# Performance work log

Hardware: AMD Instinct MI355X
Metric: run time of the kernel (lower is better)

Reference implementation:

```python
import jax, jax.numpy as jnp
import numpy as np

IMG_SHAPE = (256, 256, 256)


def _rot3(a):
    # Rx @ Ry @ Rz, matching _compute_rotation
    ax, ay, az = a[0], a[1], a[2]
    cx, sx = jnp.cos(ax), jnp.sin(ax)
    cy, sy = jnp.cos(ay), jnp.sin(ay)
    cz, sz = jnp.cos(az), jnp.sin(az)
    one = jnp.ones_like(ax)
    zero = jnp.zeros_like(ax)
    Rx = jnp.stack([jnp.stack([one, zero, zero]),
                    jnp.stack([zero, cx, -sx]),
                    jnp.stack([zero, sx, cx])])
    Ry = jnp.stack([jnp.stack([cy, zero, sy]),
                    jnp.stack([zero, one, zero]),
                    jnp.stack([-sy, zero, cy])])
    Rz = jnp.stack([jnp.stack([cz, -sz, zero]),
                    jnp.stack([sz, cz, zero]),
                    jnp.stack([zero, zero, one])])
    return Rx @ Ry @ Rz


def _rigid4(a, t, cog):
    # T_center_inv @ T_trans @ T_rot @ T_center
    R = _rot3(a)
    Tc = jnp.eye(4, dtype=a.dtype).at[:3, 3].set(-cog)
    Tci = jnp.eye(4, dtype=a.dtype).at[:3, 3].set(cog)
    Tt = jnp.eye(4, dtype=a.dtype).at[:3, 3].set(t)
    Tr = jnp.eye(4, dtype=a.dtype).at[:3, :3].set(R)
    return Tci @ Tt @ Tr @ Tc


def _trilinear(vol, di, dj, dk):
    # fast_3D_interp_torch(mode='linear'): trilinear interp, zero outside bounds
    D, H, W = vol.shape
    ok = (di >= 0) & (di <= D - 1) & (dj >= 0) & (dj <= H - 1) & (dk >= 0) & (dk <= W - 1)
    di = jnp.clip(di, 0.0, D - 1)
    dj = jnp.clip(dj, 0.0, H - 1)
    dk = jnp.clip(dk, 0.0, W - 1)
    fi = jnp.floor(di).astype(jnp.int32)
    fj = jnp.floor(dj).astype(jnp.int32)
    fk = jnp.floor(dk).astype(jnp.int32)
    ci = jnp.clip(fi + 1, 0, D - 1)
    cj = jnp.clip(fj + 1, 0, H - 1)
    ck = jnp.clip(fk + 1, 0, W - 1)
    wi = di - fi
    wj = dj - fj
    wk = dk - fk
    out = (vol[fi, fj, fk] * (1 - wi) * (1 - wj) * (1 - wk)
           + vol[fi, fj, ck] * (1 - wi) * (1 - wj) * wk
           + vol[fi, cj, fk] * (1 - wi) * wj * (1 - wk)
           + vol[fi, cj, ck] * (1 - wi) * wj * wk
           + vol[ci, fj, fk] * wi * (1 - wj) * (1 - wk)
           + vol[ci, fj, ck] * wi * (1 - wj) * wk
           + vol[ci, cj, fk] * wi * wj * (1 - wk)
           + vol[ci, cj, ck] * wi * wj * wk)
    return jnp.where(ok, out, jnp.zeros_like(out))


def setup_inputs() -> dict:
    key = jax.random.key(0)
    k1, k2 = jax.random.split(key)
    image_targ = jax.random.normal(k1, (1, 1) + IMG_SHAPE, dtype=jnp.float32)
    # small rotation so most of the warped grid stays in bounds (angle_factor=1)
    angle = 0.1 * jax.random.normal(k2, (1, 3), dtype=jnp.float32)
    translation = jnp.zeros((1, 3), dtype=jnp.float32)
    v2r = np.eye(4, dtype=np.float32)
    v2r[:3, 3] = -127.5  # center-of-volume RAS origin
    ref_v2r = jnp.asarray(v2r)
    flo_v2r = jnp.asarray(v2r)
    cog = jnp.zeros((3,), dtype=jnp.float32)
    return {"image_targ": image_targ, "angle": angle, "translation": translation,
            "ref_v2r": ref_v2r, "flo_v2r": flo_v2r, "cog": cog}


def reference(image_targ, angle, translation, ref_v2r, flo_v2r, cog):
    # tx_factor = angle_factor = 1 -> params used as-is
    T_rig = jax.vmap(lambda a, t: _rigid4(a, t, cog))(angle, translation)  # [B,4,4]
    T = (jnp.linalg.inv(flo_v2r) @ T_rig[0] @ ref_v2r).astype(jnp.float32)
    D, H, W = image_targ.shape[2:]
    gi, gj, gk = jnp.meshgrid(jnp.arange(D, dtype=jnp.float32),
                              jnp.arange(H, dtype=jnp.float32),
                              jnp.arange(W, dtype=jnp.float32), indexing='ij')
    di = T[0, 0] * gi + T[0, 1] * gj + T[0, 2] * gk + T[0, 3]
    dj = T[1, 0] * gi + T[1, 1] * gj + T[1, 2] * gk + T[1, 3]
    dk = T[2, 0] * gi + T[2, 1] * gj + T[2, 2] * gk + T[2, 3]
    image_reg = _trilinear(image_targ[0, 0], di, dj, dk)
    return image_reg[None, None]
```

## Files before the change

kernel.cpp:

```cpp
#include <hip/hip_runtime.h>
#include <math.h>

#define DD 256
#define HH 256
#define WW 256
#define TS 16
#define LDSF 16384

typedef float f2v __attribute__((ext_vector_type(2)));
typedef f2v __attribute__((aligned(4))) f2u;
typedef float f4v __attribute__((ext_vector_type(4)));
typedef f4v __attribute__((aligned(4))) f4u;

__global__ void compute_T_kernel(const float* __restrict__ angle,
                                 const float* __restrict__ trans,
                                 const float* __restrict__ ref_v2r,
                                 const float* __restrict__ flo_v2r,
                                 const float* __restrict__ cog,
                                 float* __restrict__ Tout ) {
    if (blockIdx.x != 0 || threadIdx.x != 0) return;

    const float ax = angle[0], ay = angle[1], az = angle[2];
    const float cx = cosf(ax), sx = sinf(ax);
    const float cy = cosf(ay), sy = sinf(ay);
    const float cz = cosf(az), sz = sinf(az);

    float R[3][3];
    const float a00 = cy,       a01 = 0.0f, a02 = sy;
    const float a10 = sx * sy,  a11 = cx,   a12 = -sx * cy;
    const float a20 = -cx * sy, a21 = sx,   a22 = cx * cy;
    R[0][0] = a00 * cz + a01 * sz; R[0][1] = -a00 * sz + a01 * cz; R[0][2] = a02;
    R[1][0] = a10 * cz + a11 * sz; R[1][1] = -a10 * sz + a11 * cz; R[1][2] = a12;
    R[2][0] = a20 * cz + a21 * sz; R[2][1] = -a20 * sz + a21 * cz; R[2][2] = a22;

    float Trig[4][4];
    for (int r = 0; r < 4; ++r)
        for (int c = 0; c < 4; ++c)
            Trig[r][c] = (r == c) ? 1.0f : 0.0f;
    for (int r = 0; r < 3; ++r) {
        for (int c = 0; c < 3; ++c) Trig[r][c] = R[r][c];
        Trig[r][3] = cog[r] + trans[r]
                   - (R[r][0] * cog[0] + R[r][1] * cog[1] + R[r][2] * cog[2]);
    }

    float m[16], inv[16];
    for (int q = 0; q < 16; ++q) m[q] = flo_v2r[q];
    inv[0]  =  m[5]*m[10]*m[15] - m[5]*m[11]*m[14] - m[9]*m[6]*m[15]
             + m[9]*m[7]*m[14] + m[13]*m[6]*m[11] - m[13]*m[7]*m[10];
    inv[4]  = -m[4]*m[10]*m[15] + m[4]*m[11]*m[14] + m[8]*m[6]*m[15]
             - m[8]*m[7]*m[14] - m[12]*m[6]*m[11] + m[12]*m[7]*m[10];
    inv[8]  =  m[4]*m[9]*m[15] - m[4]*m[11]*m[13] - m[8]*m[5]*m[15]
             + m[8]*m[7]*m[13] + m[12]*m[5]*m[11] - m[12]*m[7]*m[9];
    inv[12] = -m[4]*m[9]*m[14] + m[4]*m[10]*m[13] + m[8]*m[5]*m[14]
             - m[8]*m[6]*m[13] - m[12]*m[5]*m[10] + m[12]*m[6]*m[9];
    inv[1]  = -m[1]*m[10]*m[15] + m[1]*m[11]*m[14] + m[9]*m[2]*m[15]
             - m[9]*m[3]*m[14] - m[13]*m[2]*m[11] + m[13]*m[3]*m[10];
    inv[5]  =  m[0]*m[10]*m[15] - m[0]*m[11]*m[14] - m[8]*m[2]*m[15]
             + m[8]*m[3]*m[14] + m[12]*m[2]*m[11] - m[12]*m[3]*m[10];
    inv[9]  = -m[0]*m[9]*m[15] + m[0]*m[11]*m[13] + m[8]*m[1]*m[15]
             - m[8]*m[3]*m[13] - m[12]*m[1]*m[11] + m[12]*m[3]*m[9];
    inv[13] =  m[0]*m[9]*m[14] - m[0]*m[10]*m[13] - m[8]*m[1]*m[14]
             + m[8]*m[2]*m[13] + m[12]*m[1]*m[10] - m[12]*m[2]*m[9];
    inv[2]  =  m[1]*m[6]*m[15] - m[1]*m[7]*m[14] - m[5]*m[2]*m[15]
             + m[5]*m[3]*m[14] + m[13]*m[2]*m[7] - m[13]*m[3]*m[6];
    inv[6]  = -m[0]*m[6]*m[15] + m[0]*m[7]*m[14] + m[4]*m[2]*m[15]
             - m[4]*m[3]*m[14] - m[12]*m[2]*m[7] + m[12]*m[3]*m[6];
    inv[10] =  m[0]*m[5]*m[15] - m[0]*m[7]*m[13] - m[4]*m[1]*m[15]
             + m[4]*m[3]*m[13] + m[12]*m[1]*m[7] - m[12]*m[3]*m[5];
    inv[14] = -m[0]*m[5]*m[14] + m[0]*m[6]*m[13] + m[4]*m[1]*m[14]
             - m[4]*m[2]*m[13] - m[12]*m[1]*m[6] + m[12]*m[2]*m[5];
    inv[3]  = -m[1]*m[6]*m[11] + m[1]*m[7]*m[10] + m[5]*m[2]*m[11]
             - m[5]*m[3]*m[10] - m[9]*m[2]*m[7] + m[9]*m[3]*m[6];
    inv[7]  =  m[0]*m[6]*m[11] - m[0]*m[7]*m[10] - m[4]*m[2]*m[11]
             + m[4]*m[3]*m[10] + m[8]*m[2]*m[7] - m[8]*m[3]*m[6];
    inv[11] = -m[0]*m[5]*m[11] + m[0]*m[7]*m[9] + m[4]*m[1]*m[11]
             - m[4]*m[3]*m[9] - m[8]*m[1]*m[7] + m[8]*m[3]*m[5];
    inv[15] =  m[0]*m[5]*m[10] - m[0]*m[6]*m[9] - m[4]*m[1]*m[10]
             + m[4]*m[2]*m[9] + m[8]*m[1]*m[6] - m[8]*m[2]*m[5];
    const float det = m[0]*inv[0] + m[1]*inv[4] + m[2]*inv[8] + m[3]*inv[12];
    const float rdet = 1.0f / det;

    float M1[4][4];
    for (int r = 0; r < 4; ++r)
        for (int c = 0; c < 4; ++c) {
            float s = 0.0f;
            for (int q = 0; q < 4; ++q) s += Trig[r][q] * ref_v2r[q * 4 + c];
            M1[r][c] = s;
        }
    for (int r = 0; r < 3; ++r)
        for (int c = 0; c < 4; ++c) {
            float s = 0.0f;
            for (int q = 0; q < 4; ++q) s += (inv[r * 4 + q] * rdet) * M1[q][c];
            Tout[r * 4 + c] = s;
        }
}

__global__ __launch_bounds__(256) void warp_kernel(
        const float* __restrict__ vol,
        const float* __restrict__ T,
        float* __restrict__ out) {
    const float t0 = T[0],  t1 = T[1],  t2  = T[2],  t3  = T[3];
    const float t4 = T[4],  t5 = T[5],  t6  = T[6],  t7  = T[7];
    const float t8 = T[8],  t9 = T[9],  t10 = T[10], t11 = T[11];

    const int bid = blockIdx.x;
    const int xcd = bid & 7;
    const int n = bid >> 3;
    const int bi = (xcd >> 2) & 1;
    const int bj = (xcd >> 1) & 1;
    const int bk = xcd & 1;
    const int kt = n & 7;
    const int jt = (n >> 3) & 7;
    const int it = n >> 6;

    const int i0 = (bi << 7) + (it << 4);
    const int j0 = (bj << 7) + (jt << 4);
    const int k0 = (bk << 7) + (kt << 4);

    const int tid = threadIdx.x;
    const int kl = tid & 15;
    const int jl = tid >> 4;
    const int j = j0 + jl;
    const int k = k0 + kl;
    const float gj = (float)j, gk = (float)k;
    const int out_base = (i0 << 16) + (j << 8) + k;

    __shared__ float sv[LDSF];

    float mni =  1e30f, mxi = -1e30f;
    float mnj =  1e30f, mxj = -1e30f;
    float mnk =  1e30f, mxk = -1e30f;
#pragma unroll
    for (int c = 0; c < 8; ++c) {
        const float ci_ = (float)(i0 + ((c & 1) ? (TS - 1) : 0));
        const float cj_ = (float)(j0 + ((c & 2) ? (TS - 1) : 0));
        const float ck_ = (float)(k0 + ((c & 4) ? (TS - 1) : 0));
        const float di = t0 * ci_ + t1 * cj_ + t2  * ck_ + t3;
        const float dj = t4 * ci_ + t5 * cj_ + t6  * ck_ + t7;
        const float dk = t8 * ci_ + t9 * cj_ + t10 * ck_ + t11;
        mni = fminf(mni, di); mxi = fmaxf(mxi, di);
        mnj = fminf(mnj, dj); mxj = fmaxf(mxj, dj);
        mnk = fminf(mnk, dk); mxk = fmaxf(mxk, dk);
    }
    int lo_i = (int)fminf(fmaxf(mni, 0.0f), 255.0f);
    int hi_i = (int)fminf(fmaxf(mxi, 0.0f), 255.0f);
    int lo_j = (int)fminf(fmaxf(mnj, 0.0f), 255.0f);
    int hi_j = (int)fminf(fmaxf(mxj, 0.0f), 255.0f);
    int lo_k = (int)fminf(fmaxf(mnk, 0.0f), 255.0f);
    int hi_k = (int)fminf(fmaxf(mxk, 0.0f), 255.0f);
    lo_i = min(max(lo_i - 1, 0), 252);
    lo_j = min(max(lo_j - 1, 0), 252);
    lo_k = min(max(lo_k - 1, 0), 252);
    hi_i = min(max(hi_i + 2, lo_i + 3), 255);
    hi_j = min(max(hi_j + 2, lo_j + 3), 255);
    hi_k = min(max(hi_k + 2, lo_k + 3), 255);
    const int Si = hi_i - lo_i + 1;
    const int Sj = hi_j - lo_j + 1;
    const int Sk = hi_k - lo_k + 1;
    const int SjSk = Sj * Sk;
    const bool fits = (Si * SjSk <= LDSF) && (Sk <= 32);

    if (fits) {
        {
            const int kk0 = (tid & 7) << 2;
            const int rj  = tid >> 3;
            if (rj < Sj && kk0 < Sk) {
                const int kk = min(kk0, Sk - 4);
                const float* gp = vol + ((lo_i << 16) + ((lo_j + rj) << 8)
                                         + lo_k + kk);
                float* sp = sv + rj * Sk + kk;
                for (int li = 0; li < Si; ++li, gp += 65536, sp += SjSk) {
                    const f4v p = *(const f4u*)gp;
                    *(f4u*)sp = p;
                }
            }
        }
        __syncthreads();

#pragma unroll
        for (int IT = 0; IT < 4; ++IT) {
            const float gi_ = (float)(i0 + IT * 4);
            float di_ = t0 * gi_ + t1 * gj + t2  * gk + t3;
            float dj_ = t4 * gi_ + t5 * gj + t6  * gk + t7;
            float dk_ = t8 * gi_ + t9 * gj + t10 * gk + t11;
#pragma unroll
            for (int s_ = 0; s_ < 4; ++s_) {
                const float cdi = fminf(fmaxf(di_, 0.0f), (float)(DD - 1));
                const float cdj = fminf(fmaxf(dj_, 0.0f), (float)(HH - 1));
                const float cdk = fminf(fmaxf(dk_, 0.0f), (float)(WW - 1));
                const int fi = (int)cdi;
                const int fj = (int)cdj;
                const int fk = (int)cdk;
                const int ci = min(fi + 1, DD - 1);
                const int cj = min(fj + 1, HH - 1);
                const int pk = min(fk, WW - 2);
                const float wi = cdi - (float)fi;
                const float wj = cdj - (float)fj;
                const float wk = cdk - (float)pk;
                const bool ok_ = (di_ >= 0.0f) & (di_ <= (float)(DD - 1)) &
                                 (dj_ >= 0.0f) & (dj_ <= (float)(HH - 1)) &
                                 (dk_ >= 0.0f) & (dk_ <= (float)(WW - 1));

                const int o_fi = (fi - lo_i) * SjSk;
                const int o_ci = (ci - lo_i) * SjSk;
                const int o_fj = (fj - lo_j) * Sk;
                const int o_cj = (cj - lo_j) * Sk;
                const int pl = pk - lo_k;

                const f2v v0 = *(const f2u*)(sv + o_fi + o_fj + pl);
                const f2v v1 = *(const f2u*)(sv + o_fi + o_cj + pl);
                const f2v v2 = *(const f2u*)(sv + o_ci + o_fj + pl);
                const f2v v3 = *(const f2u*)(sv + o_ci + o_cj + pl);

                const float c00 = v0.x + (v0.y - v0.x) * wk;
                const float c01 = v1.x + (v1.y - v1.x) * wk;
                const float c10 = v2.x + (v2.y - v2.x) * wk;
                const float c11 = v3.x + (v3.y - v3.x) * wk;
                const float c0  = c00 + (c01 - c00) * wj;
                const float c1  = c10 + (c11 - c10) * wj;
                const float val = c0 + (c1 - c0) * wi;

                __builtin_nontemporal_store(ok_ ? val : 0.0f,
                    &out[out_base + ((IT * 4 + s_) << 16)]);

                di_ += t0; dj_ += t4; dk_ += t8;
            }
        }
    } else {
#pragma unroll
        for (int IT = 0; IT < 4; ++IT) {
            const float gi_ = (float)(i0 + IT * 4);
            float di_ = t0 * gi_ + t1 * gj + t2  * gk + t3;
            float dj_ = t4 * gi_ + t5 * gj + t6  * gk + t7;
            float dk_ = t8 * gi_ + t9 * gj + t10 * gk + t11;
#pragma unroll
            for (int s_ = 0; s_ < 4; ++s_) {
                const float cdi = fminf(fmaxf(di_, 0.0f), (float)(DD - 1));
                const float cdj = fminf(fmaxf(dj_, 0.0f), (float)(HH - 1));
                const float cdk = fminf(fmaxf(dk_, 0.0f), (float)(WW - 1));
                const int fi = (int)cdi;
                const int fj = (int)cdj;
                const int fk = (int)cdk;
                const int ci = min(fi + 1, DD - 1);
                const int cj = min(fj + 1, HH - 1);
                const int pk = min(fk, WW - 2);
                const float wi = cdi - (float)fi;
                const float wj = cdj - (float)fj;
                const float wk = cdk - (float)pk;
                const bool ok_ = (di_ >= 0.0f) & (di_ <= (float)(DD - 1)) &
                                 (dj_ >= 0.0f) & (dj_ <= (float)(HH - 1)) &
                                 (dk_ >= 0.0f) & (dk_ <= (float)(WW - 1));

                const int fi_o = fi << 16, ci_o = ci << 16;
                const int fj_o = fj << 8,  cj_o = cj << 8;
                const f2v v0 = *(const f2u*)(vol + (fi_o + fj_o + pk));
                const f2v v1 = *(const f2u*)(vol + (fi_o + cj_o + pk));
                const f2v v2 = *(const f2u*)(vol + (ci_o + fj_o + pk));
                const f2v v3 = *(const f2u*)(vol + (ci_o + cj_o + pk));

                const float c00 = v0.x + (v0.y - v0.x) * wk;
                const float c01 = v1.x + (v1.y - v1.x) * wk;
                const float c10 = v2.x + (v2.y - v2.x) * wk;
                const float c11 = v3.x + (v3.y - v3.x) * wk;
                const float c0  = c00 + (c01 - c00) * wj;
                const float c1  = c10 + (c11 - c10) * wj;
                const float val = c0 + (c1 - c0) * wi;

                __builtin_nontemporal_store(ok_ ? val : 0.0f,
                    &out[out_base + ((IT * 4 + s_) << 16)]);

                di_ += t0; dj_ += t4; dk_ += t8;
            }
        }
    }
}

extern "C" void kernel_launch(void* const* d_in, const int* in_sizes, int n_in,
                              void* d_out, int out_size, void* d_ws, size_t ws_size,
                              hipStream_t stream) {
    const float* image_targ  = (const float*)d_in[0];
    const float* angle       = (const float*)d_in[1];
    const float* translation = (const float*)d_in[2];
    const float* ref_v2r     = (const float*)d_in[3];
    const float* flo_v2r     = (const float*)d_in[4];
    const float* cog         = (const float*)d_in[5];
    float* out = (float*)d_out;
    float* Tws = (float*)d_ws;

    compute_T_kernel<<<1, 64, 0, stream>>>(angle, translation, ref_v2r,
                                           flo_v2r, cog, Tws);
    warp_kernel<<<(DD / TS) * (HH / TS) * (WW / TS), 256, 0, stream>>>(
        image_targ, Tws, out);
}
```

Baseline: 199.5 us.

## Shrink warp tile to 16x8x16 with padded LDS rows and parallel staging

```diff
diff --git a/kernel.cpp b/kernel.cpp
--- a/kernel.cpp
+++ b/kernel.cpp
@@ -4,8 +4,10 @@
 #define DD 256
 #define HH 256
 #define WW 256
-#define TS 16
-#define LDSF 16384
+#define TI 16
+#define TJ 8
+#define TK 16
+#define LDSF 8192
 
 typedef float f2v __attribute__((ext_vector_type(2)));
 typedef f2v __attribute__((aligned(4))) f2u;
@@ -110,16 +112,17 @@
     const int bj = (xcd >> 1) & 1;
     const int bk = xcd & 1;
     const int kt = n & 7;
-    const int jt = (n >> 3) & 7;
-    const int it = n >> 6;
+    const int jt = (n >> 3) & 15;
+    const int it = n >> 7;
 
     const int i0 = (bi << 7) + (it << 4);
-    const int j0 = (bj << 7) + (jt << 4);
+    const int j0 = (bj << 7) + (jt << 3);
     const int k0 = (bk << 7) + (kt << 4);
 
     const int tid = threadIdx.x;
     const int kl = tid & 15;
-    const int jl = tid >> 4;
+    const int jl = (tid >> 4) & 7;
+    const int ihalf = tid >> 7;
     const int j = j0 + jl;
     const int k = k0 + kl;
     const float gj = (float)j, gk = (float)k;
@@ -132,9 +135,9 @@
     float mnk =  1e30f, mxk = -1e30f;
 #pragma unroll
     for (int c = 0; c < 8; ++c) {
-        const float ci_ = (float)(i0 + ((c & 1) ? (TS - 1) : 0));
-        const float cj_ = (float)(j0 + ((c & 2) ? (TS - 1) : 0));
-        const float ck_ = (float)(k0 + ((c & 4) ? (TS - 1) : 0));
+        const float ci_ = (float)(i0 + ((c & 1) ? (TI - 1) : 0));
+        const float cj_ = (float)(j0 + ((c & 2) ? (TJ - 1) : 0));
+        const float ck_ = (float)(k0 + ((c & 4) ? (TK - 1) : 0));
         const float di = t0 * ci_ + t1 * cj_ + t2  * ck_ + t3;
         const float dj = t4 * ci_ + t5 * cj_ + t6  * ck_ + t7;
         const float dk = t8 * ci_ + t9 * cj_ + t10 * ck_ + t11;
@@ -156,30 +159,49 @@
     hi_k = min(max(hi_k + 2, lo_k + 3), 255);
     const int Si = hi_i - lo_i + 1;
     const int Sj = hi_j - lo_j + 1;
-    const int Sk = hi_k - lo_k + 1;
-    const int SjSk = Sj * Sk;
-    const bool fits = (Si * SjSk <= LDSF) && (Sk <= 32);
+    int Sk  = hi_k - lo_k + 1;
+    int SkL = (Sk + 3) & ~3;
+    if (lo_k + SkL > 256) {
+        lo_k = 256 - SkL;
+        Sk = hi_k - lo_k + 1;
+        SkL = (Sk + 3) & ~3;
+    }
+    int Pk = SkL;
+    if ((Pk & 7) == 0) Pk += 4;
+    const int SjPk = Sj * Pk;
+    const bool fits = (Si * SjPk <= LDSF) && (Sj <= 16) && (Sk <= 32);
 
     if (fits) {
         {
-            const int kk0 = (tid & 7) << 2;
-            const int rj  = tid >> 3;
-            if (rj < Sj && kk0 < Sk) {
-                const int kk = min(kk0, Sk - 4);
-                const float* gp = vol + ((lo_i << 16) + ((lo_j + rj) << 8)
-                                         + lo_k + kk);
-                float* sp = sv + rj * Sk + kk;
-                for (int li = 0; li < Si; ++li, gp += 65536, sp += SjSk) {
-                    const f4v p = *(const f4u*)gp;
-                    *(f4u*)sp = p;
+            const int lj  = tid & 15;
+            const int c4  = (tid >> 4) & 7;
+            const int li0 = tid >> 7;
+            const int kk  = c4 << 2;
+            if (lj < Sj && kk < SkL) {
+                const float* gp = vol + ((lo_i + li0) << 16)
+                                      + ((lo_j + lj) << 8) + lo_k + kk;
+                float* sp = sv + (li0 * Sj + lj) * Pk + kk;
+                int li = li0;
+                for (; li + 2 < Si; li += 4) {
+                    const f4v a = *(const f4u*)gp;
+                    const f4v b = *(const f4u*)(gp + (2 << 16));
+                    *(f4u*)sp = a;
+                    *(f4u*)(sp + 2 * SjPk) = b;
+                    gp += 4 << 16;
+                    sp += 4 * SjPk;
+                }
+                for (; li < Si; li += 2) {
+                    *(f4u*)sp = *(const f4u*)gp;
+                    gp += 2 << 16;
+                    sp += 2 * SjPk;
                 }
             }
         }
         __syncthreads();
 
 #pragma unroll
-        for (int IT = 0; IT < 4; ++IT) {
-            const float gi_ = (float)(i0 + IT * 4);
+        for (int IT = 0; IT < 2; ++IT) {
+            const float gi_ = (float)(i0 + ihalf * 8 + IT * 4);
             float di_ = t0 * gi_ + t1 * gj + t2  * gk + t3;
             float dj_ = t4 * gi_ + t5 * gj + t6  * gk + t7;
             float dk_ = t8 * gi_ + t9 * gj + t10 * gk + t11;
@@ -201,10 +223,10 @@
                                  (dj_ >= 0.0f) & (dj_ <= (float)(HH - 1)) &
                                  (dk_ >= 0.0f) & (dk_ <= (float)(WW - 1));
 
-                const int o_fi = (fi - lo_i) * SjSk;
-                const int o_ci = (ci - lo_i) * SjSk;
-                const int o_fj = (fj - lo_j) * Sk;
-                const int o_cj = (cj - lo_j) * Sk;
+                const int o_fi = (fi - lo_i) * SjPk;
+                const int o_ci = (ci - lo_i) * SjPk;
+                const int o_fj = (fj - lo_j) * Pk;
+                const int o_cj = (cj - lo_j) * Pk;
                 const int pl = pk - lo_k;
 
                 const f2v v0 = *(const f2u*)(sv + o_fi + o_fj + pl);
@@ -221,15 +243,15 @@
                 const float val = c0 + (c1 - c0) * wi;
 
                 __builtin_nontemporal_store(ok_ ? val : 0.0f,
-                    &out[out_base + ((IT * 4 + s_) << 16)]);
+                    &out[out_base + ((ihalf * 8 + IT * 4 + s_) << 16)]);
 
                 di_ += t0; dj_ += t4; dk_ += t8;
             }
         }
     } else {
 #pragma unroll
-        for (int IT = 0; IT < 4; ++IT) {
-            const float gi_ = (float)(i0 + IT * 4);
+        for (int IT = 0; IT < 2; ++IT) {
+            const float gi_ = (float)(i0 + ihalf * 8 + IT * 4);
             float di_ = t0 * gi_ + t1 * gj + t2  * gk + t3;
             float dj_ = t4 * gi_ + t5 * gj + t6  * gk + t7;
             float dk_ = t8 * gi_ + t9 * gj + t10 * gk + t11;
@@ -267,7 +289,7 @@
                 const float val = c0 + (c1 - c0) * wi;
 
                 __builtin_nontemporal_store(ok_ ? val : 0.0f,
-                    &out[out_base + ((IT * 4 + s_) << 16)]);
+                    &out[out_base + ((ihalf * 8 + IT * 4 + s_) << 16)]);
 
                 di_ += t0; dj_ += t4; dk_ += t8;
             }
@@ -289,6 +311,6 @@
 
     compute_T_kernel<<<1, 64, 0, stream>>>(angle, translation, ref_v2r,
                                            flo_v2r, cog, Tws);
-    warp_kernel<<<(DD / TS) * (HH / TS) * (WW / TS), 256, 0, stream>>>(
+    warp_kernel<<<(DD / TI) * (HH / TJ) * (WW / TK), 256, 0, stream>>>(
         image_targ, Tws, out);
 }
```

Result: faster. 170.4 us (-14.6%).
